# Optimization experiments

Measured on AMD Instinct MI355X. Metric: run time of the kernel, lower is better.

## Reference

```python
import jax, jax.numpy as jnp
import numpy as np

NEG = -9e15
SLOPE = 0.02

def setup_inputs() -> dict:
    key = jax.random.key(0)
    k1, k2, k3, k4 = jax.random.split(key, 4)
    N, IN, OUT = 16384, 128, 64
    x = jax.random.normal(k1, (N, IN), dtype=jnp.float32)
    adj = jax.random.randint(k2, (N, N), 0, 2, dtype=jnp.int32)
    weight = jax.random.normal(k3, (IN, OUT), dtype=jnp.float32) * (1.0 / np.sqrt(IN))
    att_weight = jax.random.normal(k4, (2 * OUT, 1), dtype=jnp.float32) * (1.0 / np.sqrt(2 * OUT))
    return {"x": x, "adj": adj, "weight": weight, "att_weight": att_weight}

def reference(x, adj, weight, att_weight):
    out_feature = weight.shape[1]
    Wh = x @ weight                                   # [N, out]
    f_i = Wh @ att_weight[:out_feature, :]            # [N, 1] source term
    f_j = Wh @ att_weight[out_feature:, :]            # [N, 1] dest term
    e = f_i + f_j.T                                   # [N, N] additive scores
    e = jax.nn.leaky_relu(e, negative_slope=SLOPE)
    att = jnp.where(adj > 0, e, NEG)
    att = jax.nn.softmax(att, axis=1)                 # masked row softmax
    h_prime = att @ Wh                                # [N, out]
    return jax.nn.elu(h_prime)                        # concat=True -> elu
```

## Files before the change

### kernel.cpp

```cpp
#include <hip/hip_runtime.h>
#include <cstdint>
#include <cstddef>

#define GN   16384
#define GIN  128
#define GOUT 64
#define NCH  8
#define LOG2E 1.44269504088896340736f

typedef __attribute__((ext_vector_type(8))) short short8;
typedef __attribute__((ext_vector_type(4))) float f32x4;
typedef __attribute__((ext_vector_type(4))) int   int4v;

__device__ __forceinline__ unsigned short f2bf(float f) {
  unsigned u = __float_as_uint(f);
  return (unsigned short)((u + 0x8000u) >> 16);
}

__device__ __forceinline__ unsigned short f2bf_rne(float f) {
  unsigned u = __float_as_uint(f);
  u += 0x7FFFu + ((u >> 16) & 1u);
  return (unsigned short)(u >> 16);
}

__global__ __launch_bounds__(256) void prep_kernel(
    const float* __restrict__ x, const float* __restrict__ w,
    const float* __restrict__ aw, unsigned short* __restrict__ wpk,
    float* __restrict__ fs2, float* __restrict__ fd2)
{
  __shared__ float ws[GIN * GOUT];
  __shared__ float red[2][64][4];

  const int t = threadIdx.x;
  const int rb = blockIdx.x * 64;

  for (int i = t; i < (GIN * GOUT) / 4; i += 256)
    ((float4*)ws)[i] = ((const float4*)w)[i];
  __syncthreads();

  const int r = t & 63, s = t >> 6;
  const int row = rb + r;
  const float* xr = x + (size_t)row * GIN;

  float acc[16];
#pragma unroll
  for (int d = 0; d < 16; ++d) acc[d] = 0.f;

  for (int kk = 0; kk < GIN; kk += 4) {
    float4 xv = *(const float4*)(xr + kk);
    float xa[4] = {xv.x, xv.y, xv.z, xv.w};
#pragma unroll
    for (int u = 0; u < 4; ++u) {
#pragma unroll
      for (int d = 0; d < 16; ++d)
        acc[d] += xa[u] * ws[(kk + u) * GOUT + s * 16 + d];
    }
  }

  const int jc = row >> 5;
  const int qq = (row & 31) >> 3;
  const int tt = row & 7;
  float psrc = 0.f, pdst = 0.f;
#pragma unroll
  for (int d = 0; d < 16; ++d) {
    const int dg = s * 16 + d;
    psrc += acc[d] * aw[dg];
    pdst += acc[d] * aw[GOUT + dg];
    const int f = dg >> 4, n = dg & 15;
    wpk[(size_t)jc * 4096 + f * 1024 + (qq * 16 + n) * 8 + tt] = f2bf_rne(acc[d]);
  }
  red[0][r][s] = psrc;
  red[1][r][s] = pdst;
  __syncthreads();
  if (s == 0) {
    float a_ = red[0][r][0] + red[0][r][1] + red[0][r][2] + red[0][r][3];
    float b_ = red[1][r][0] + red[1][r][1] + red[1][r][2] + red[1][r][3];
    fs2[row] = a_ * LOG2E;
    fd2[row] = b_ * LOG2E;
  }
}

__global__ __launch_bounds__(256, 2) void gat_main(
    const int* __restrict__ adj, const unsigned short* __restrict__ wpk,
    const float* __restrict__ fs2, const float* __restrict__ fd2,
    float* __restrict__ nump, float* __restrict__ denp)
{
  __shared__ unsigned mk[4][32][66];

  const int w    = threadIdx.x >> 6;
  const int lane = threadIdx.x & 63;
  const int br    = blockIdx.x & 127;
  const int chunk = blockIdx.x >> 7;
  const int strip32 = br * 4 + w;
  const int m = lane & 15;
  const int q = lane >> 4;
  const int q8 = q << 3;

  const int CW = GN / NCH;
  const int j0 = chunk * CW;

  {
    const int4v* ap = (const int4v*)(adj + (size_t)(strip32 * 32) * GN + j0);
    const int lane8 = lane * 8;
#pragma unroll 1
    for (int r = 0; r < 32; ++r) {
      unsigned bits = 0;
#pragma unroll
      for (int k = 0; k < 8; ++k) {
        int4v v = ap[lane8 + k];
        bits |= ((unsigned)(v.x != 0) << (k * 4))
              | ((unsigned)(v.y != 0) << (k * 4 + 1))
              | ((unsigned)(v.z != 0) << (k * 4 + 2))
              | ((unsigned)(v.w != 0) << (k * 4 + 3));
      }
      mk[w][r][lane] = bits;
      ap += GN / 4;
    }
  }
  __syncthreads();

  const int row0 = strip32 * 32 + m;
  const int row1 = row0 + 16;
  const float fs0 = fs2[row0];
  const float fs1 = fs2[row1];

  const float4* __restrict__ fdv  = (const float4*)fd2;
  const short8* __restrict__ wpk8 = (const short8*)wpk;

  f32x4 acc0[4], acc1[4];
  f32x4 accd0, accd1;
  accd0 = accd1 = (f32x4){0.f, 0.f, 0.f, 0.f};
#pragma unroll
  for (int b = 0; b < 4; ++b) {
    acc0[b] = (f32x4){0.f, 0.f, 0.f, 0.f};
    acc1[b] = (f32x4){0.f, 0.f, 0.f, 0.f};
  }

  short8 b_ones;
#pragma unroll
  for (int i = 0; i < 8; ++i) b_ones[i] = (short)0x3F80;

  auto pelem = [&](unsigned byte, int t, float fd, float fsv) -> unsigned short {
    float sv = fsv + fd;
    float lv = fmaxf(sv, 0.02f * sv);
    float pe = __builtin_amdgcn_exp2f(lv);
    pe = (byte & (1u << t)) ? pe : 0.f;
    return f2bf(pe);
  };

  auto mk_af = [&](unsigned byte, float4 fA, float4 fB, float fsv) -> short8 {
    short8 af;
    af[0] = (short)pelem(byte, 0, fA.x, fsv);
    af[1] = (short)pelem(byte, 1, fA.y, fsv);
    af[2] = (short)pelem(byte, 2, fA.z, fsv);
    af[3] = (short)pelem(byte, 3, fA.w, fsv);
    af[4] = (short)pelem(byte, 4, fB.x, fsv);
    af[5] = (short)pelem(byte, 5, fB.y, fsv);
    af[6] = (short)pelem(byte, 6, fB.z, fsv);
    af[7] = (short)pelem(byte, 7, fB.w, fsv);
    return af;
  };

#pragma unroll 1
  for (int j = j0; j < j0 + CW; j += 32) {
    const int i4 = (j >> 2) + (q << 1);
    const int wi = (j - j0) >> 5;

    const unsigned w0 = mk[w][m][wi];
    const unsigned w1 = mk[w][m + 16][wi];
    const float4 f0 = fdv[i4];
    const float4 f1 = fdv[i4 + 1];

    const short8* wb = wpk8 + (size_t)(j >> 5) * 512 + lane;
    const short8 b0 = wb[0];
    const short8 b1 = wb[128];
    const short8 b2 = wb[256];
    const short8 b3 = wb[384];

    {
      const unsigned byte = (w0 >> q8) & 0xffu;
      short8 af = mk_af(byte, f0, f1, fs0);
      acc0[0] = __builtin_amdgcn_mfma_f32_16x16x32_bf16(af, b0, acc0[0], 0, 0, 0);
      acc0[1] = __builtin_amdgcn_mfma_f32_16x16x32_bf16(af, b1, acc0[1], 0, 0, 0);
      acc0[2] = __builtin_amdgcn_mfma_f32_16x16x32_bf16(af, b2, acc0[2], 0, 0, 0);
      acc0[3] = __builtin_amdgcn_mfma_f32_16x16x32_bf16(af, b3, acc0[3], 0, 0, 0);
      accd0   = __builtin_amdgcn_mfma_f32_16x16x32_bf16(af, b_ones, accd0, 0, 0, 0);
    }
    {
      const unsigned byte = (w1 >> q8) & 0xffu;
      short8 af = mk_af(byte, f0, f1, fs1);
      acc1[0] = __builtin_amdgcn_mfma_f32_16x16x32_bf16(af, b0, acc1[0], 0, 0, 0);
      acc1[1] = __builtin_amdgcn_mfma_f32_16x16x32_bf16(af, b1, acc1[1], 0, 0, 0);
      acc1[2] = __builtin_amdgcn_mfma_f32_16x16x32_bf16(af, b2, acc1[2], 0, 0, 0);
      acc1[3] = __builtin_amdgcn_mfma_f32_16x16x32_bf16(af, b3, acc1[3], 0, 0, 0);
      accd1   = __builtin_amdgcn_mfma_f32_16x16x32_bf16(af, b_ones, accd1, 0, 0, 0);
    }
  }

  float* np = nump + (size_t)chunk * GN * GOUT;
  float* dp = denp + (size_t)chunk * GN;
  {
    const int orow0 = strip32 * 32 + q * 4;
#pragma unroll
    for (int r = 0; r < 4; ++r) {
      float* nr = np + (size_t)(orow0 + r) * GOUT + m;
      __builtin_nontemporal_store(acc0[0][r], nr + 0);
      __builtin_nontemporal_store(acc0[1][r], nr + 16);
      __builtin_nontemporal_store(acc0[2][r], nr + 32);
      __builtin_nontemporal_store(acc0[3][r], nr + 48);
      if (m == 0) dp[orow0 + r] = accd0[r];
    }
  }
  {
    const int orow0 = strip32 * 32 + 16 + q * 4;
#pragma unroll
    for (int r = 0; r < 4; ++r) {
      float* nr = np + (size_t)(orow0 + r) * GOUT + m;
      __builtin_nontemporal_store(acc1[0][r], nr + 0);
      __builtin_nontemporal_store(acc1[1][r], nr + 16);
      __builtin_nontemporal_store(acc1[2][r], nr + 32);
      __builtin_nontemporal_store(acc1[3][r], nr + 48);
      if (m == 0) dp[orow0 + r] = accd1[r];
    }
  }
}

__global__ __launch_bounds__(256) void fin_kernel(
    const float* __restrict__ nump, const float* __restrict__ denp,
    float* __restrict__ out)
{
  const int g = blockIdx.x * 256 + threadIdx.x;
  if (g >= GN * GOUT) return;
  const int row = g >> 6;
  float s = 0.f, d = 0.f;
#pragma unroll
  for (int c = 0; c < NCH; ++c) {
    s += nump[(size_t)c * GN * GOUT + g];
    d += denp[(size_t)c * GN + row];
  }
  float v = s / d;
  out[g] = (v > 0.f) ? v : expm1f(v);
}

extern "C" void kernel_launch(void* const* d_in, const int* in_sizes, int n_in,
                              void* d_out, int out_size, void* d_ws, size_t ws_size,
                              hipStream_t stream) {
  const float* x   = (const float*)d_in[0];
  const int*   adj = (const int*)d_in[1];
  const float* w   = (const float*)d_in[2];
  const float* aw  = (const float*)d_in[3];
  float* out = (float*)d_out;

  float* nump = (float*)d_ws;
  float* denp = nump + (size_t)NCH * GN * GOUT;
  float* fs2  = denp + (size_t)NCH * GN;
  float* fd2  = fs2 + GN;
  unsigned short* wpk = (unsigned short*)(fd2 + GN);

  prep_kernel<<<GN / 64, 256, 0, stream>>>(x, w, aw, wpk, fs2, fd2);
  gat_main<<<(GN / 128) * NCH, 256, 0, stream>>>(adj, wpk, fs2, fd2, nump, denp);
  fin_kernel<<<(GN * GOUT) / 256, 256, 0, stream>>>(nump, denp, out);
}
```

Baseline: 1.398 ms.

## Stage adjacency mask in double-buffered sub-chunks interleaved with MFMA compute

The adjacency bitmask build is split from one up-front pass over 2048 columns into four 512-column stages. The stages are double-buffered in shared memory and staged between compute phases, so streaming the large int32 adjacency matrix mixes with MFMA work across waves instead of forming one serial load phase. The block-wide barrier goes away because each wave only reads the mask it wrote itself. Adjacency loads become nontemporal, and the smaller LDS footprint lets launch bounds request three blocks per CU for more latency hiding. The cost is extra register pressure from the higher occupancy target and a staging step that is still synchronous within each wave.

```diff
diff --git a/kernel.cpp b/kernel.cpp
--- a/kernel.cpp
+++ b/kernel.cpp
@@ -80,12 +80,12 @@
   }
 }
 
-__global__ __launch_bounds__(256, 2) void gat_main(
+__global__ __launch_bounds__(256, 3) void gat_main(
     const int* __restrict__ adj, const unsigned short* __restrict__ wpk,
     const float* __restrict__ fs2, const float* __restrict__ fd2,
     float* __restrict__ nump, float* __restrict__ denp)
 {
-  __shared__ unsigned mk[4][32][66];
+  __shared__ unsigned mk[2][4][32][17];
 
   const int w    = threadIdx.x >> 6;
   const int lane = threadIdx.x & 63;
@@ -99,25 +99,27 @@
   const int CW = GN / NCH;
   const int j0 = chunk * CW;
 
-  {
-    const int4v* ap = (const int4v*)(adj + (size_t)(strip32 * 32) * GN + j0);
-    const int lane8 = lane * 8;
-#pragma unroll 1
-    for (int r = 0; r < 32; ++r) {
+  const int colwin = lane & 15;
+  const int rb4 = lane >> 4;
+  auto STAGE = [&](int buf, int s) {
+    const int4v* bp = (const int4v*)(adj + (size_t)(strip32 * 32) * GN
+                                     + j0 + s * 512 + colwin * 32);
+#pragma unroll
+    for (int it = 0; it < 8; ++it) {
+      const int r = it * 4 + rb4;
+      const int4v* p = bp + (size_t)r * (GN / 4);
       unsigned bits = 0;
 #pragma unroll
       for (int k = 0; k < 8; ++k) {
-        int4v v = ap[lane8 + k];
+        int4v v = __builtin_nontemporal_load(p + k);
         bits |= ((unsigned)(v.x != 0) << (k * 4))
               | ((unsigned)(v.y != 0) << (k * 4 + 1))
               | ((unsigned)(v.z != 0) << (k * 4 + 2))
               | ((unsigned)(v.w != 0) << (k * 4 + 3));
       }
-      mk[w][r][lane] = bits;
-      ap += GN / 4;
-    }
-  }
-  __syncthreads();
+      mk[buf][w][r][colwin] = bits;
+    }
+  };
 
   const int row0 = strip32 * 32 + m;
   const int row1 = row0 + 16;
@@ -161,40 +163,49 @@
     return af;
   };
 
+  STAGE(0, 0);
+
 #pragma unroll 1
-  for (int j = j0; j < j0 + CW; j += 32) {
-    const int i4 = (j >> 2) + (q << 1);
-    const int wi = (j - j0) >> 5;
-
-    const unsigned w0 = mk[w][m][wi];
-    const unsigned w1 = mk[w][m + 16][wi];
-    const float4 f0 = fdv[i4];
-    const float4 f1 = fdv[i4 + 1];
-
-    const short8* wb = wpk8 + (size_t)(j >> 5) * 512 + lane;
-    const short8 b0 = wb[0];
-    const short8 b1 = wb[128];
-    const short8 b2 = wb[256];
-    const short8 b3 = wb[384];
-
-    {
-      const unsigned byte = (w0 >> q8) & 0xffu;
-      short8 af = mk_af(byte, f0, f1, fs0);
-      acc0[0] = __builtin_amdgcn_mfma_f32_16x16x32_bf16(af, b0, acc0[0], 0, 0, 0);
-      acc0[1] = __builtin_amdgcn_mfma_f32_16x16x32_bf16(af, b1, acc0[1], 0, 0, 0);
-      acc0[2] = __builtin_amdgcn_mfma_f32_16x16x32_bf16(af, b2, acc0[2], 0, 0, 0);
-      acc0[3] = __builtin_amdgcn_mfma_f32_16x16x32_bf16(af, b3, acc0[3], 0, 0, 0);
-      accd0   = __builtin_amdgcn_mfma_f32_16x16x32_bf16(af, b_ones, accd0, 0, 0, 0);
-    }
-    {
-      const unsigned byte = (w1 >> q8) & 0xffu;
-      short8 af = mk_af(byte, f0, f1, fs1);
-      acc1[0] = __builtin_amdgcn_mfma_f32_16x16x32_bf16(af, b0, acc1[0], 0, 0, 0);
-      acc1[1] = __builtin_amdgcn_mfma_f32_16x16x32_bf16(af, b1, acc1[1], 0, 0, 0);
-      acc1[2] = __builtin_amdgcn_mfma_f32_16x16x32_bf16(af, b2, acc1[2], 0, 0, 0);
-      acc1[3] = __builtin_amdgcn_mfma_f32_16x16x32_bf16(af, b3, acc1[3], 0, 0, 0);
-      accd1   = __builtin_amdgcn_mfma_f32_16x16x32_bf16(af, b_ones, accd1, 0, 0, 0);
-    }
+  for (int s = 0; s < 4; ++s) {
+    const int buf = s & 1;
+    const int jb = j0 + s * 512;
+#pragma unroll 1
+    for (int jj = 0; jj < 512; jj += 32) {
+      const int j = jb + jj;
+      const int i4 = (j >> 2) + (q << 1);
+      const int wi = jj >> 5;
+
+      const unsigned w0 = mk[buf][w][m][wi];
+      const unsigned w1 = mk[buf][w][m + 16][wi];
+      const float4 f0 = fdv[i4];
+      const float4 f1 = fdv[i4 + 1];
+
+      const short8* wb = wpk8 + (size_t)(j >> 5) * 512 + lane;
+      const short8 b0 = wb[0];
+      const short8 b1 = wb[128];
+      const short8 b2 = wb[256];
+      const short8 b3 = wb[384];
+
+      {
+        const unsigned byte = (w0 >> q8) & 0xffu;
+        short8 af = mk_af(byte, f0, f1, fs0);
+        acc0[0] = __builtin_amdgcn_mfma_f32_16x16x32_bf16(af, b0, acc0[0], 0, 0, 0);
+        acc0[1] = __builtin_amdgcn_mfma_f32_16x16x32_bf16(af, b1, acc0[1], 0, 0, 0);
+        acc0[2] = __builtin_amdgcn_mfma_f32_16x16x32_bf16(af, b2, acc0[2], 0, 0, 0);
+        acc0[3] = __builtin_amdgcn_mfma_f32_16x16x32_bf16(af, b3, acc0[3], 0, 0, 0);
+        accd0   = __builtin_amdgcn_mfma_f32_16x16x32_bf16(af, b_ones, accd0, 0, 0, 0);
+      }
+      {
+        const unsigned byte = (w1 >> q8) & 0xffu;
+        short8 af = mk_af(byte, f0, f1, fs1);
+        acc1[0] = __builtin_amdgcn_mfma_f32_16x16x32_bf16(af, b0, acc1[0], 0, 0, 0);
+        acc1[1] = __builtin_amdgcn_mfma_f32_16x16x32_bf16(af, b1, acc1[1], 0, 0, 0);
+        acc1[2] = __builtin_amdgcn_mfma_f32_16x16x32_bf16(af, b2, acc1[2], 0, 0, 0);
+        acc1[3] = __builtin_amdgcn_mfma_f32_16x16x32_bf16(af, b3, acc1[3], 0, 0, 0);
+        accd1   = __builtin_amdgcn_mfma_f32_16x16x32_bf16(af, b_ones, accd1, 0, 0, 0);
+      }
+    }
+    if (s < 3) STAGE(buf ^ 1, s + 1);
   }
 
   float* np = nump + (size_t)chunk * GN * GOUT;
```

Result: slower. 1.743 ms (+24.7%).
